# Performance work log

Measured on AMD Instinct MI355X. Metric: run time of the kernel, lower is better.

## Reference

```python
import jax, jax.numpy as jnp
import numpy as np

NUM_CLASS = 22  # restypes_with_x_and_gap


def setup_inputs() -> dict:
    key = jax.random.key(0)
    k1, k2, k3, k4 = jax.random.split(key, 4)
    b, m, n, c = 1, 128, 256, NUM_CLASS
    variant = jax.random.randint(k1, (b, m, n), 0, c)              # int variant sequences
    variant_mask = jnp.ones((b, m, n), dtype=jnp.float32)
    eij = jax.random.normal(k2, (b, n, n, c, c), dtype=jnp.float32) * 0.1  # Potts couplings wij
    ei = jax.random.normal(k3, (b, n, c), dtype=jnp.float32) * 0.1         # fields bi
    mask_vec = jnp.ones((c,), dtype=jnp.float32).at[-1].set(0.0)   # mask out gap '-' class
    sigma = jnp.ones((1,), dtype=jnp.float32)                      # prior_w=1.0, task_num=1
    return {"variant": variant, "variant_mask": variant_mask, "eij": eij,
            "ei": ei, "mask_vec": mask_vec, "sigma": sigma}


def reference(variant, variant_mask, eij, ei, mask_vec, sigma):
    c = mask_vec.shape[0]
    onehot = jax.nn.one_hot(variant, c, dtype=eij.dtype)           # [b,m,n,c]
    # fold class mask into couplings, then Potts energy per position/class
    em = eij * mask_vec                                            # [b,i,j,c,d]
    hi = jnp.einsum('bmjd,bijcd->bmic', onehot, em)                # [b,m,i,c]
    motifs = ei[:, None] + hi                                      # [b,m,i,c]
    # log_softmax=False branch: pick the logit of the active class per position
    logits = jnp.einsum('bmic,bmic->bmi', motifs, onehot)          # [b,m,i]
    # eval path: delta vs reference variant (index 0), sum-pooled, scaled by sigma
    vm = variant_mask[..., None]                                   # [b,m,i,1]
    vm = vm * vm[:, :1]
    vlogit = logits - logits[:, :1]                                # [b,m,i]
    pooled = jnp.sum(vlogit[..., None] * vm, axis=-2)              # [b,m,task_num]
    variant_logit = sigma * pooled
    return motifs, logits, variant_logit
```

## Files before the change

### kernel.cpp

```cpp
#include <hip/hip_runtime.h>

#define NC    22
#define NROW  (NC*NC)
#define NJ    256
#define NI    256
#define NM    128
#define JG    8
#define NQJ   4
#define JQ    (NJ/NQJ)
#define SS    (JQ/JG)
#define ROWDW 16
#define JROW  (NC*ROWDW)
#define TILEDW (JG*JROW)
#define F4PS  (JG*NROW/4)

typedef __attribute__((ext_vector_type(8))) short short8;
typedef __attribute__((ext_vector_type(4))) float f32x4;

__device__ inline uint32_t bf16rne(float x) {
    uint32_t u = __float_as_uint(x);
    u += 0x7FFFu + ((u >> 16) & 1u);
    return u >> 16;
}

__global__ __launch_bounds__(256) void potts_mfma(
    const int*   __restrict__ variant,
    const float* __restrict__ eij,
    const float* __restrict__ mask_vec,
    float*       __restrict__ part)
{
    const int i    = blockIdx.x;
    const int jq   = blockIdx.y;
    const int tid  = threadIdx.x;
    const int lane = tid & 63;
    const int wv   = tid >> 6;
    const int q    = lane >> 4;
    const int nl   = lane & 15;

    __shared__ uint32_t tile[2][TILEDW];
    __shared__ int      vtab[2][JG][NM];

    for (int p = tid; p < 2 * JG * NC * 5; p += 256) {
        const int b  = p / (JG * NC * 5), r = p % (JG * NC * 5);
        const int jl = r / (NC * 5),     r2 = r % (NC * 5);
        tile[b][jl * JROW + (r2 / 5) * ROWDW + 11 + r2 % 5] = 0;
    }

    int   l0[4], l1[4];
    float mk[4][4];
    bool  act[4];
    #pragma unroll
    for (int r = 0; r < 4; ++r) {
        const int f4 = r * 256 + tid;
        act[r] = (f4 < F4PS);
        const int fc = act[r] ? f4 : 0;
        const int jl = fc / 121, r4 = fc % 121;
        const int f2a = 2 * r4, f2b = f2a + 1;
        const int ca = f2a / 11, wa = f2a % 11;
        const int cb = f2b / 11, wb = f2b % 11;
        l0[r] = jl * JROW + ca * ROWDW + wa;
        l1[r] = jl * JROW + cb * ROWDW + wb;
        mk[r][0] = mask_vec[2 * wa];  mk[r][1] = mask_vec[2 * wa + 1];
        mk[r][2] = mask_vec[2 * wb];  mk[r][3] = mask_vec[2 * wb + 1];
    }

    const float4* gsrc = (const float4*)eij + (size_t)(i * NJ + jq * JQ) * 121;

    const int c1   = 16 + nl;
    const int off0 = nl * ROWDW + q * 4;
    const int off1 = (c1 < NC ? c1 : 0) * ROWDW + q * 4;
    const int m0a  = wv * 16;
    const int m0b  = wv * 16 + 64;

    f32x4 acc_a0 = {0.f,0.f,0.f,0.f}, acc_a1 = {0.f,0.f,0.f,0.f};
    f32x4 acc_b0 = {0.f,0.f,0.f,0.f}, acc_b1 = {0.f,0.f,0.f,0.f};

    float4 pf[4];
    int    vr[4];
    #pragma unroll
    for (int r = 0; r < 4; ++r)
        if (act[r]) pf[r] = gsrc[r * 256 + tid];
    #pragma unroll
    for (int r = 0; r < 4; ++r) {
        const int t = r * 256 + tid;
        vr[r] = variant[(t >> 3) * NJ + jq * JQ + (t & 7)];
    }

    for (int s = 0; s < SS; ++s) {
        const int bsel = s & 1;
        uint32_t* buf = tile[bsel];

        #pragma unroll
        for (int r = 0; r < 4; ++r) {
            if (act[r]) {
                const float4 v = pf[r];
                buf[l0[r]] = bf16rne(v.x * mk[r][0])
                           | (bf16rne(v.y * mk[r][1]) << 16);
                buf[l1[r]] = bf16rne(v.z * mk[r][2])
                           | (bf16rne(v.w * mk[r][3]) << 16);
            }
        }
        #pragma unroll
        for (int r = 0; r < 4; ++r) {
            const int t = r * 256 + tid;
            vtab[bsel][t & 7][t >> 3] = vr[r];
        }
        __syncthreads();

        if (s + 1 < SS) {
            const float4* gn = gsrc + (size_t)(s + 1) * F4PS;
            #pragma unroll
            for (int r = 0; r < 4; ++r)
                if (act[r]) pf[r] = gn[r * 256 + tid];
            #pragma unroll
            for (int r = 0; r < 4; ++r) {
                const int t = r * 256 + tid;
                vr[r] = variant[(t >> 3) * NJ + jq * JQ + (s + 1) * JG + (t & 7)];
            }
        }

        #pragma unroll
        for (int jl = 0; jl < JG; ++jl) {
            const uint32_t* jrow = buf + jl * JROW;
            const short8 bf0 = *(const short8*)(jrow + off0);
            const short8 bf1 = *(const short8*)(jrow + off1);

            const int va = vtab[bsel][jl][m0a + nl];
            const int vb = vtab[bsel][jl][m0b + nl];

            const uint32_t pa = 0x3F80u << ((va & 1) << 4);
            const uint32_t pb = 0x3F80u << ((vb & 1) << 4);
            const int ha = va >> 1, hb = vb >> 1, kb = q * 4;
            union { uint32_t u[4]; short8 s; } fa, fb;
            #pragma unroll
            for (int t = 0; t < 4; ++t) {
                fa.u[t] = (ha == kb + t) ? pa : 0u;
                fb.u[t] = (hb == kb + t) ? pb : 0u;
            }

            acc_a0 = __builtin_amdgcn_mfma_f32_16x16x32_bf16(fa.s, bf0, acc_a0, 0, 0, 0);
            acc_a1 = __builtin_amdgcn_mfma_f32_16x16x32_bf16(fa.s, bf1, acc_a1, 0, 0, 0);
            acc_b0 = __builtin_amdgcn_mfma_f32_16x16x32_bf16(fb.s, bf0, acc_b0, 0, 0, 0);
            acc_b1 = __builtin_amdgcn_mfma_f32_16x16x32_bf16(fb.s, bf1, acc_b1, 0, 0, 0);
        }
    }

    float* pbase = part + ((size_t)jq * NI + i) * NM * NC;
    #pragma unroll
    for (int t = 0; t < 4; ++t) {
        const int ra = m0a + q * 4 + t, rb = m0b + q * 4 + t;
        pbase[ra * NC + nl] = acc_a0[t];
        pbase[rb * NC + nl] = acc_b0[t];
        if (c1 < NC) {
            pbase[ra * NC + c1] = acc_a1[t];
            pbase[rb * NC + c1] = acc_b1[t];
        }
    }
}

__global__ __launch_bounds__(256) void potts_reduce(
    const float* __restrict__ part,
    const int*   __restrict__ variant,
    const float* __restrict__ ei,
    float*       __restrict__ out_motifs,
    float*       __restrict__ out_logits)
{
    const int i    = blockIdx.x;
    const int tid  = threadIdx.x;
    const int m    = tid & 127;
    const int half = tid >> 7;
    const int cc0  = half * 11;

    const float* p0 = part + (((size_t)0 * NI + i) * NM + m) * NC + cc0;
    const float* p1 = part + (((size_t)1 * NI + i) * NM + m) * NC + cc0;
    const float* p2 = part + (((size_t)2 * NI + i) * NM + m) * NC + cc0;
    const float* p3 = part + (((size_t)3 * NI + i) * NM + m) * NC + cc0;
    const float* eirow = ei + i * NC;
    float* mout = out_motifs + ((size_t)m * NI + i) * NC;
    const int vi = variant[m * NJ + i];

    float logit = 0.f;
    #pragma unroll
    for (int k = 0; k < 11; ++k) {
        const float v = p0[k] + p1[k] + p2[k] + p3[k] + eirow[cc0 + k];
        mout[cc0 + k] = v;
        if (cc0 + k == vi) logit = v;
    }
    if (vi >= cc0 && vi < cc0 + 11)
        out_logits[m * NI + i] = logit;
}

__global__ __launch_bounds__(64) void potts_pool(
    const float* __restrict__ logits,
    const float* __restrict__ vmask,
    const float* __restrict__ sigma,
    float*       __restrict__ out_vl)
{
    const int m    = blockIdx.x;
    const int lane = threadIdx.x;
    float s = 0.f;
    #pragma unroll
    for (int qq = 0; qq < 4; ++qq) {
        const int i = lane + 64 * qq;
        const float vl = logits[m * NI + i] - logits[i];
        s += vl * vmask[m * NI + i] * vmask[i];
    }
    #pragma unroll
    for (int off = 32; off > 0; off >>= 1)
        s += __shfl_down(s, off, 64);
    if (lane == 0) out_vl[m] = sigma[0] * s;
}

extern "C" void kernel_launch(void* const* d_in, const int* in_sizes, int n_in,
                              void* d_out, int out_size, void* d_ws, size_t ws_size,
                              hipStream_t stream) {
    const int*   variant  = (const int*)  d_in[0];
    const float* vmask    = (const float*)d_in[1];
    const float* eij      = (const float*)d_in[2];
    const float* ei       = (const float*)d_in[3];
    const float* mask_vec = (const float*)d_in[4];
    const float* sigma    = (const float*)d_in[5];

    float* out        = (float*)d_out;
    float* out_motifs = out;
    float* out_logits = out_motifs + NM * NI * NC;
    float* out_vl     = out_logits + NM * NI;

    float* part = (float*)d_ws;

    dim3 gridA(NI, NQJ);
    potts_mfma<<<gridA, 256, 0, stream>>>(variant, eij, mask_vec, part);
    potts_reduce<<<NI, 256, 0, stream>>>(part, variant, ei,
                                         out_motifs, out_logits);
    potts_pool<<<NM, 64, 0, stream>>>(out_logits, vmask, sigma, out_vl);
}
```

Measured before the change: 201.2 us.

## Fuse Potts MFMA and reduce into one kernel with direct-to-LDS async loads

```diff
diff --git a/kernel.cpp b/kernel.cpp
--- a/kernel.cpp
+++ b/kernel.cpp
@@ -1,193 +1,149 @@
 #include <hip/hip_runtime.h>
 
 #define NC    22
-#define NROW  (NC*NC)
+#define NI    256
 #define NJ    256
-#define NI    256
 #define NM    128
 #define JG    8
-#define NQJ   4
-#define JQ    (NJ/NQJ)
-#define SS    (JQ/JG)
-#define ROWDW 16
-#define JROW  (NC*ROWDW)
-#define TILEDW (JG*JROW)
-#define F4PS  (JG*NROW/4)
+#define NSS   (NJ/JG)
+#define SLOT  512
+#define MOTLD 23
 
 typedef __attribute__((ext_vector_type(8))) short short8;
 typedef __attribute__((ext_vector_type(4))) float f32x4;
 
-__device__ inline uint32_t bf16rne(float x) {
+__device__ __forceinline__ uint32_t bf16rne(float x) {
     uint32_t u = __float_as_uint(x);
     u += 0x7FFFu + ((u >> 16) & 1u);
     return u >> 16;
 }
 
-__global__ __launch_bounds__(256) void potts_mfma(
+__device__ __forceinline__ uint32_t pk_bf16(float lo, float hi) {
+    uint32_t r;
+    asm("v_cvt_pk_bf16_f32 %0, %1, %2" : "=v"(r) : "v"(lo), "v"(hi));
+    return r;
+}
+
+__device__ __forceinline__ void gload_lds16(const void* g, void* l) {
+    __builtin_amdgcn_global_load_lds(
+        (const __attribute__((address_space(1))) void*)g,
+        (__attribute__((address_space(3))) void*)l, 16, 0, 0);
+}
+
+union u32x4s8 { uint32_t u[4]; short8 s; };
+
+__global__ __launch_bounds__(1024) void potts_fused(
     const int*   __restrict__ variant,
     const float* __restrict__ eij,
+    const float* __restrict__ ei,
     const float* __restrict__ mask_vec,
-    float*       __restrict__ part)
-{
-    const int i    = blockIdx.x;
-    const int jq   = blockIdx.y;
-    const int tid  = threadIdx.x;
-    const int lane = tid & 63;
-    const int wv   = tid >> 6;
-    const int q    = lane >> 4;
-    const int nl   = lane & 15;
-
-    __shared__ uint32_t tile[2][TILEDW];
-    __shared__ int      vtab[2][JG][NM];
-
-    for (int p = tid; p < 2 * JG * NC * 5; p += 256) {
-        const int b  = p / (JG * NC * 5), r = p % (JG * NC * 5);
-        const int jl = r / (NC * 5),     r2 = r % (NC * 5);
-        tile[b][jl * JROW + (r2 / 5) * ROWDW + 11 + r2 % 5] = 0;
-    }
-
-    int   l0[4], l1[4];
-    float mk[4][4];
-    bool  act[4];
-    #pragma unroll
-    for (int r = 0; r < 4; ++r) {
-        const int f4 = r * 256 + tid;
-        act[r] = (f4 < F4PS);
-        const int fc = act[r] ? f4 : 0;
-        const int jl = fc / 121, r4 = fc % 121;
-        const int f2a = 2 * r4, f2b = f2a + 1;
-        const int ca = f2a / 11, wa = f2a % 11;
-        const int cb = f2b / 11, wb = f2b % 11;
-        l0[r] = jl * JROW + ca * ROWDW + wa;
-        l1[r] = jl * JROW + cb * ROWDW + wb;
-        mk[r][0] = mask_vec[2 * wa];  mk[r][1] = mask_vec[2 * wa + 1];
-        mk[r][2] = mask_vec[2 * wb];  mk[r][3] = mask_vec[2 * wb + 1];
-    }
-
-    const float4* gsrc = (const float4*)eij + (size_t)(i * NJ + jq * JQ) * 121;
-
-    const int c1   = 16 + nl;
-    const int off0 = nl * ROWDW + q * 4;
-    const int off1 = (c1 < NC ? c1 : 0) * ROWDW + q * 4;
-    const int m0a  = wv * 16;
-    const int m0b  = wv * 16 + 64;
-
-    f32x4 acc_a0 = {0.f,0.f,0.f,0.f}, acc_a1 = {0.f,0.f,0.f,0.f};
-    f32x4 acc_b0 = {0.f,0.f,0.f,0.f}, acc_b1 = {0.f,0.f,0.f,0.f};
-
-    float4 pf[4];
-    int    vr[4];
-    #pragma unroll
-    for (int r = 0; r < 4; ++r)
-        if (act[r]) pf[r] = gsrc[r * 256 + tid];
-    #pragma unroll
-    for (int r = 0; r < 4; ++r) {
-        const int t = r * 256 + tid;
-        vr[r] = variant[(t >> 3) * NJ + jq * JQ + (t & 7)];
-    }
-
-    for (int s = 0; s < SS; ++s) {
-        const int bsel = s & 1;
-        uint32_t* buf = tile[bsel];
-
-        #pragma unroll
-        for (int r = 0; r < 4; ++r) {
-            if (act[r]) {
-                const float4 v = pf[r];
-                buf[l0[r]] = bf16rne(v.x * mk[r][0])
-                           | (bf16rne(v.y * mk[r][1]) << 16);
-                buf[l1[r]] = bf16rne(v.z * mk[r][2])
-                           | (bf16rne(v.w * mk[r][3]) << 16);
-            }
-        }
-        #pragma unroll
-        for (int r = 0; r < 4; ++r) {
-            const int t = r * 256 + tid;
-            vtab[bsel][t & 7][t >> 3] = vr[r];
-        }
-        __syncthreads();
-
-        if (s + 1 < SS) {
-            const float4* gn = gsrc + (size_t)(s + 1) * F4PS;
-            #pragma unroll
-            for (int r = 0; r < 4; ++r)
-                if (act[r]) pf[r] = gn[r * 256 + tid];
-            #pragma unroll
-            for (int r = 0; r < 4; ++r) {
-                const int t = r * 256 + tid;
-                vr[r] = variant[(t >> 3) * NJ + jq * JQ + (s + 1) * JG + (t & 7)];
-            }
-        }
-
-        #pragma unroll
-        for (int jl = 0; jl < JG; ++jl) {
-            const uint32_t* jrow = buf + jl * JROW;
-            const short8 bf0 = *(const short8*)(jrow + off0);
-            const short8 bf1 = *(const short8*)(jrow + off1);
-
-            const int va = vtab[bsel][jl][m0a + nl];
-            const int vb = vtab[bsel][jl][m0b + nl];
-
-            const uint32_t pa = 0x3F80u << ((va & 1) << 4);
-            const uint32_t pb = 0x3F80u << ((vb & 1) << 4);
-            const int ha = va >> 1, hb = vb >> 1, kb = q * 4;
-            union { uint32_t u[4]; short8 s; } fa, fb;
-            #pragma unroll
-            for (int t = 0; t < 4; ++t) {
-                fa.u[t] = (ha == kb + t) ? pa : 0u;
-                fb.u[t] = (hb == kb + t) ? pb : 0u;
-            }
-
-            acc_a0 = __builtin_amdgcn_mfma_f32_16x16x32_bf16(fa.s, bf0, acc_a0, 0, 0, 0);
-            acc_a1 = __builtin_amdgcn_mfma_f32_16x16x32_bf16(fa.s, bf1, acc_a1, 0, 0, 0);
-            acc_b0 = __builtin_amdgcn_mfma_f32_16x16x32_bf16(fb.s, bf0, acc_b0, 0, 0, 0);
-            acc_b1 = __builtin_amdgcn_mfma_f32_16x16x32_bf16(fb.s, bf1, acc_b1, 0, 0, 0);
-        }
-    }
-
-    float* pbase = part + ((size_t)jq * NI + i) * NM * NC;
-    #pragma unroll
-    for (int t = 0; t < 4; ++t) {
-        const int ra = m0a + q * 4 + t, rb = m0b + q * 4 + t;
-        pbase[ra * NC + nl] = acc_a0[t];
-        pbase[rb * NC + nl] = acc_b0[t];
-        if (c1 < NC) {
-            pbase[ra * NC + c1] = acc_a1[t];
-            pbase[rb * NC + c1] = acc_b1[t];
-        }
-    }
-}
-
-__global__ __launch_bounds__(256) void potts_reduce(
-    const float* __restrict__ part,
-    const int*   __restrict__ variant,
-    const float* __restrict__ ei,
     float*       __restrict__ out_motifs,
     float*       __restrict__ out_logits)
 {
     const int i    = blockIdx.x;
     const int tid  = threadIdx.x;
-    const int m    = tid & 127;
-    const int half = tid >> 7;
-    const int cc0  = half * 11;
+    const int lane = tid & 63;
+    const int w    = tid >> 6;
+    const int jl   = w >> 1;
+    const int mh   = w & 1;
+    const int q    = lane >> 4;
+    const int nl   = lane & 15;
+    const int c1   = 16 + nl;
 
-    const float* p0 = part + (((size_t)0 * NI + i) * NM + m) * NC + cc0;
-    const float* p1 = part + (((size_t)1 * NI + i) * NM + m) * NC + cc0;
-    const float* p2 = part + (((size_t)2 * NI + i) * NM + m) * NC + cc0;
-    const float* p3 = part + (((size_t)3 * NI + i) * NM + m) * NC + cc0;
+    __shared__ float    tile[2][JG][SLOT];
+    __shared__ int      vtab[2][NM * JG];
+    __shared__ uint32_t maskTab[32];
+
+    if (tid < 32) maskTab[tid] = (tid < NC) ? bf16rne(mask_vec[tid]) : 0u;
+    if (tid < 2 * JG * (SLOT - 484)) {
+        const int b = tid / (JG * 28), r = tid % (JG * 28);
+        tile[b][r / 28][484 + (r % 28)] = 0.f;
+    }
+
+    const int    poff  = mh ? 228 : 0;
+    const size_t ebase = ((size_t)i * NJ + jl) * 484 + poff + lane * 4;
+    const bool vstage = (w >= 8) && ((w & 1) == 0);
+    const int  pidx   = (w - 8) >> 1;
+    const int  vmrow  = (pidx * 32 + (lane >> 1)) * NJ + (lane & 1) * 4;
+
+    gload_lds16(eij + ebase, &tile[0][jl][poff]);
+    if (vstage) gload_lds16(variant + vmrow, &vtab[0][pidx * 256]);
+
+    f32x4 acc[4][2];
+    #pragma unroll
+    for (int mt = 0; mt < 4; ++mt) {
+        acc[mt][0] = (f32x4){0.f, 0.f, 0.f, 0.f};
+        acc[mt][1] = (f32x4){0.f, 0.f, 0.f, 0.f};
+    }
+
+    for (int s = 0; s < NSS; ++s) {
+        const int cur = s & 1;
+        __syncthreads();
+        if (s + 1 < NSS) {
+            const int nxt = cur ^ 1;
+            gload_lds16(eij + ebase + (size_t)(s + 1) * (JG * 484),
+                        &tile[nxt][jl][poff]);
+            if (vstage)
+                gload_lds16(variant + vmrow + (s + 1) * JG,
+                            &vtab[nxt][pidx * 256]);
+        }
+
+        const float* jrow = &tile[cur][jl][0];
+        const float* r0 = jrow + nl * NC + q * 8;
+        const float* r1 = jrow + (c1 < NC ? c1 : 0) * NC + q * 8;
+        const float2 x0 = *(const float2*)(r0 + 0);
+        const float2 x1 = *(const float2*)(r0 + 2);
+        const float2 x2 = *(const float2*)(r0 + 4);
+        const float2 x3 = *(const float2*)(r0 + 6);
+        const float2 y0 = *(const float2*)(r1 + 0);
+        const float2 y1 = *(const float2*)(r1 + 2);
+        const float2 y2 = *(const float2*)(r1 + 4);
+        const float2 y3 = *(const float2*)(r1 + 6);
+        u32x4s8 B0, B1;
+        B0.u[0] = pk_bf16(x0.x, x0.y);  B0.u[1] = pk_bf16(x1.x, x1.y);
+        B0.u[2] = pk_bf16(x2.x, x2.y);  B0.u[3] = pk_bf16(x3.x, x3.y);
+        B1.u[0] = pk_bf16(y0.x, y0.y);  B1.u[1] = pk_bf16(y1.x, y1.y);
+        B1.u[2] = pk_bf16(y2.x, y2.y);  B1.u[3] = pk_bf16(y3.x, y3.y);
+
+        const int* vt = vtab[cur];
+        const int  kb = q * 4;
+        #pragma unroll
+        for (int mt = 0; mt < 4; ++mt) {
+            const int      va = vt[(mh * 64 + mt * 16 + nl) * JG + jl] & 31;
+            const uint32_t pa = maskTab[va] << ((va & 1) << 4);
+            const int      ha = va >> 1;
+            u32x4s8 A;
+            #pragma unroll
+            for (int t = 0; t < 4; ++t) A.u[t] = (ha == kb + t) ? pa : 0u;
+            acc[mt][0] = __builtin_amdgcn_mfma_f32_16x16x32_bf16(A.s, B0.s, acc[mt][0], 0, 0, 0);
+            acc[mt][1] = __builtin_amdgcn_mfma_f32_16x16x32_bf16(A.s, B1.s, acc[mt][1], 0, 0, 0);
+        }
+    }
+
+    __syncthreads();
+    float* mot = &tile[0][0][0];
+    for (int p = tid; p < NM * MOTLD; p += 1024) mot[p] = 0.f;
+    __syncthreads();
+    #pragma unroll
+    for (int mt = 0; mt < 4; ++mt) {
+        #pragma unroll
+        for (int t = 0; t < 4; ++t) {
+            const int row = mh * 64 + mt * 16 + q * 4 + t;
+            atomicAdd(&mot[row * MOTLD + nl], acc[mt][0][t]);
+            if (c1 < NC) atomicAdd(&mot[row * MOTLD + c1], acc[mt][1][t]);
+        }
+    }
+    __syncthreads();
     const float* eirow = ei + i * NC;
-    float* mout = out_motifs + ((size_t)m * NI + i) * NC;
-    const int vi = variant[m * NJ + i];
-
-    float logit = 0.f;
-    #pragma unroll
-    for (int k = 0; k < 11; ++k) {
-        const float v = p0[k] + p1[k] + p2[k] + p3[k] + eirow[cc0 + k];
-        mout[cc0 + k] = v;
-        if (cc0 + k == vi) logit = v;
+    for (int p = tid; p < NM * 32; p += 1024) {
+        const int m = p >> 5, c = p & 31;
+        if (c < NC)
+            out_motifs[((size_t)m * NI + i) * NC + c] = mot[m * MOTLD + c] + eirow[c];
     }
-    if (vi >= cc0 && vi < cc0 + 11)
-        out_logits[m * NI + i] = logit;
+    if (tid < NM) {
+        const int vi = variant[tid * NJ + i];
+        out_logits[tid * NI + i] = mot[tid * MOTLD + vi] + eirow[vi];
+    }
 }
 
 __global__ __launch_bounds__(64) void potts_pool(
@@ -226,11 +182,7 @@
     float* out_logits = out_motifs + NM * NI * NC;
     float* out_vl     = out_logits + NM * NI;
 
-    float* part = (float*)d_ws;
-
-    dim3 gridA(NI, NQJ);
-    potts_mfma<<<gridA, 256, 0, stream>>>(variant, eij, mask_vec, part);
-    potts_reduce<<<NI, 256, 0, stream>>>(part, variant, ei,
+    potts_fused<<<NI, 1024, 0, stream>>>(variant, eij, ei, mask_vec,
                                          out_motifs, out_logits);
     potts_pool<<<NM, 64, 0, stream>>>(out_logits, vmask, sigma, out_vl);
 }
```

Result: slower. 234.2 us (+16.5%).

## Split j-range into eight slabs, use packed bf16 convert, flatten reduce kernel

Applied to the files above, without the earlier changes.

```diff
diff --git a/kernel.cpp b/kernel.cpp
--- a/kernel.cpp
+++ b/kernel.cpp
@@ -6,21 +6,22 @@
 #define NI    256
 #define NM    128
 #define JG    8
-#define NQJ   4
+#define NQJ   8
 #define JQ    (NJ/NQJ)
 #define SS    (JQ/JG)
 #define ROWDW 16
 #define JROW  (NC*ROWDW)
 #define TILEDW (JG*JROW)
 #define F4PS  (JG*NROW/4)
+#define SLAB  (NI*NM*NC)
 
 typedef __attribute__((ext_vector_type(8))) short short8;
 typedef __attribute__((ext_vector_type(4))) float f32x4;
 
-__device__ inline uint32_t bf16rne(float x) {
-    uint32_t u = __float_as_uint(x);
-    u += 0x7FFFu + ((u >> 16) & 1u);
-    return u >> 16;
+__device__ __forceinline__ uint32_t pk_bf16(float lo, float hi) {
+    uint32_t r;
+    asm("v_cvt_pk_bf16_f32 %0, %1, %2" : "=v"(r) : "v"(lo), "v"(hi));
+    return r;
 }
 
 __global__ __launch_bounds__(256) void potts_mfma(
@@ -94,10 +95,8 @@
         for (int r = 0; r < 4; ++r) {
             if (act[r]) {
                 const float4 v = pf[r];
-                buf[l0[r]] = bf16rne(v.x * mk[r][0])
-                           | (bf16rne(v.y * mk[r][1]) << 16);
-                buf[l1[r]] = bf16rne(v.z * mk[r][2])
-                           | (bf16rne(v.w * mk[r][3]) << 16);
+                buf[l0[r]] = pk_bf16(v.x * mk[r][0], v.y * mk[r][1]);
+                buf[l1[r]] = pk_bf16(v.z * mk[r][2], v.w * mk[r][3]);
             }
         }
         #pragma unroll
@@ -158,36 +157,28 @@
     }
 }
 
-__global__ __launch_bounds__(256) void potts_reduce(
+__global__ __launch_bounds__(1024) void potts_reduce(
     const float* __restrict__ part,
     const int*   __restrict__ variant,
     const float* __restrict__ ei,
     float*       __restrict__ out_motifs,
     float*       __restrict__ out_logits)
 {
-    const int i    = blockIdx.x;
-    const int tid  = threadIdx.x;
-    const int m    = tid & 127;
-    const int half = tid >> 7;
-    const int cc0  = half * 11;
-
-    const float* p0 = part + (((size_t)0 * NI + i) * NM + m) * NC + cc0;
-    const float* p1 = part + (((size_t)1 * NI + i) * NM + m) * NC + cc0;
-    const float* p2 = part + (((size_t)2 * NI + i) * NM + m) * NC + cc0;
-    const float* p3 = part + (((size_t)3 * NI + i) * NM + m) * NC + cc0;
-    const float* eirow = ei + i * NC;
-    float* mout = out_motifs + ((size_t)m * NI + i) * NC;
-    const int vi = variant[m * NJ + i];
-
-    float logit = 0.f;
-    #pragma unroll
-    for (int k = 0; k < 11; ++k) {
-        const float v = p0[k] + p1[k] + p2[k] + p3[k] + eirow[cc0 + k];
-        mout[cc0 + k] = v;
-        if (cc0 + k == vi) logit = v;
-    }
-    if (vi >= cc0 && vi < cc0 + 11)
-        out_logits[m * NI + i] = logit;
+    const int idx = blockIdx.x * 1024 + threadIdx.x;
+    float s = 0.f;
+    #pragma unroll
+    for (int qq = 0; qq < NQJ; ++qq)
+        s += part[(size_t)qq * SLAB + idx];
+
+    const int i = idx / (NM * NC);
+    const int r = idx - i * (NM * NC);
+    const int m = r / NC;
+    const int c = r - m * NC;
+
+    const float v = s + ei[i * NC + c];
+    out_motifs[((size_t)m * NI + i) * NC + c] = v;
+    if (c == variant[m * NJ + i])
+        out_logits[m * NI + i] = v;
 }
 
 __global__ __launch_bounds__(64) void potts_pool(
@@ -230,7 +221,7 @@
 
     dim3 gridA(NI, NQJ);
     potts_mfma<<<gridA, 256, 0, stream>>>(variant, eij, mask_vec, part);
-    potts_reduce<<<NI, 256, 0, stream>>>(part, variant, ei,
-                                         out_motifs, out_logits);
+    potts_reduce<<<SLAB / 1024, 1024, 0, stream>>>(part, variant, ei,
+                                                   out_motifs, out_logits);
     potts_pool<<<NM, 64, 0, stream>>>(out_logits, vmask, sigma, out_vl);
 }
```

Result: slower. 208.8 us (+3.8%).
